# Kernel tuning notes

Measured on AMD Instinct MI355X. Metric: run time of the kernel, lower is better.

Reference implementation:

```python
import jax, jax.numpy as jnp
import numpy as np

H = 1024   # hidden_dim
B = 4096   # batch
T = 128    # forecast_len
IN = 1     # output_dim (univariate)


def setup_inputs() -> dict:
    key = jax.random.key(0)
    ks = jax.random.split(key, 8)
    s = 1.0 / np.sqrt(H)  # torch LSTM/Linear default uniform init scale
    u = lambda k, shape: jax.random.uniform(k, shape, jnp.float32, -s, s)
    return {
        "hidden": jax.random.normal(ks[0], (1, B, H), jnp.float32),
        "cell":   jax.random.normal(ks[1], (1, B, H), jnp.float32),
        "W_ih":   u(ks[2], (4 * H, IN)),   # torch gate order: i, f, g, o
        "W_hh":   u(ks[3], (4 * H, H)),
        "b_ih":   u(ks[4], (4 * H,)),
        "b_hh":   u(ks[5], (4 * H,)),
        "W_out":  u(ks[6], (IN, H)),
        "b_out":  u(ks[7], (IN,)),
    }


def reference(hidden, cell, W_ih, W_hh, b_ih, b_hh, W_out, b_out):
    h = hidden[0]  # [B, H]  (num_layers == 1)
    c = cell[0]    # [B, H]
    x0 = jnp.zeros((h.shape[0], IN), h.dtype)  # initial decoder input = zeros
    b = b_ih + b_hh

    def step(carry, _):
        x, h, c = carry
        gates = x @ W_ih.T + h @ W_hh.T + b          # [B, 4H]
        i, f, g, o = jnp.split(gates, 4, axis=-1)    # torch order i,f,g,o
        c = jax.nn.sigmoid(f) * c + jax.nn.sigmoid(i) * jnp.tanh(g)
        h = jax.nn.sigmoid(o) * jnp.tanh(c)
        pred = h @ W_out.T + b_out                   # [B, 1]
        return (pred, h, c), pred                    # prediction fed back as next input

    _, preds = jax.lax.scan(step, (x0, h, c), None, length=T)  # [T, B, 1]
    return jnp.transpose(preds, (1, 0, 2))  # [B, T, 1]
```

## Files before the change

### kernel.cpp

```cpp
#include <hip/hip_runtime.h>
#include <hip/hip_bf16.h>
#include <stdint.h>


#define HH 1024
#define BB 4096
#define TT 128

#define BM 128
#define BJ 32
#define BKK 64

typedef __bf16 bf16;
typedef __bf16 v8bf __attribute__((ext_vector_type(8)));
typedef float f32x4 __attribute__((ext_vector_type(4)));

__device__ __forceinline__ float fast_sigmoid(float x) {
    return 1.0f / (1.0f + __expf(-x));
}
__device__ __forceinline__ float fast_tanh(float x) {
    return 1.0f - 2.0f / (__expf(2.0f * x) + 1.0f);
}

__device__ __forceinline__ void gload_lds16(const void* g, void* l) {
    __builtin_amdgcn_global_load_lds(
        (const __attribute__((address_space(1))) uint32_t*)(uintptr_t)g,
        (__attribute__((address_space(3))) uint32_t*)(uint32_t)(uintptr_t)l,
        16, 0, 0);
}


__global__ void prep_weights(const float* __restrict__ Whh,
                             const float* __restrict__ bih,
                             const float* __restrict__ bhh,
                             bf16* __restrict__ Wr,
                             float* __restrict__ bias) {
    int idx = blockIdx.x * blockDim.x + threadIdx.x;
    if (idx < 4 * HH * HH) {
        int k   = idx & (HH - 1);
        int row = idx >> 10;
        int jb  = row >> 7;
        int g   = (row >> 5) & 3;
        int jj  = row & 31;
        int srow = g * HH + jb * 32 + jj;
        Wr[idx] = (bf16)Whh[srow * HH + k];
    }
    if (idx < 4 * HH) bias[idx] = bih[idx] + bhh[idx];
}

__global__ void prep_h(const float* __restrict__ h0, bf16* __restrict__ hb) {
    int idx = blockIdx.x * blockDim.x + threadIdx.x;
    if (idx < BB * HH) hb[idx] = (bf16)h0[idx];
}

__global__ void prep_pred(float* __restrict__ predbuf, const float* __restrict__ b_out) {
    int idx = blockIdx.x * blockDim.x + threadIdx.x;
    if (idx < (TT + 1) * BB) predbuf[idx] = (idx < BB) ? 0.0f : b_out[0];
}


__global__ __launch_bounds__(256, 4)
void lstm_step(const bf16* __restrict__ hread, bf16* __restrict__ hwrite,
               const float* __restrict__ cin, float* __restrict__ cout,
               const bf16* __restrict__ Wr, const float* __restrict__ bias,
               const float* __restrict__ Wih, const float* __restrict__ Wout,
               const float* __restrict__ predbuf_r, float* __restrict__ predbuf_w) {
    __shared__ bf16 As[BM][BKK];
    __shared__ bf16 Bs[BM][BKK];

    const int tid   = threadIdx.x;
    const int lane  = tid & 63;
    const int w     = tid >> 6;
    const int waveM = w >> 1, waveN = w & 1;
    const int quad  = lane >> 4, l15 = lane & 15;

    const int bid    = blockIdx.x;
    const int jb     = (bid & 7) * 4 + ((bid >> 3) & 3);
    const int blockB = (bid >> 5) * BM;

    f32x4 acc[4][4];
#pragma unroll
    for (int mi = 0; mi < 4; mi++)
#pragma unroll
        for (int g = 0; g < 4; g++) acc[mi][g] = (f32x4){0.f, 0.f, 0.f, 0.f};

    const bf16* Asrc = hread + (size_t)blockB * HH;
    const bf16* Bsrc = Wr + (size_t)jb * 128 * HH;

    const int r8 = lane >> 3;
    const int gc = (lane & 7) ^ r8;
    const int swr = l15 & 7;

    for (int k0 = 0; k0 < HH; k0 += BKK) {
#pragma unroll
        for (int c2 = 0; c2 < 4; c2++) {
            const int rowb = w * 32 + c2 * 8;
            gload_lds16(Asrc + (size_t)(rowb + r8) * HH + k0 + gc * 8, &As[rowb][0]);
            gload_lds16(Bsrc + (size_t)(rowb + r8) * HH + k0 + gc * 8, &Bs[rowb][0]);
        }
        asm volatile("s_waitcnt vmcnt(0)" ::: "memory");
        __syncthreads();
#pragma unroll
        for (int kk = 0; kk < 2; kk++) {
            v8bf a[4], b[4];
            const int pch = ((kk * 4 + quad) ^ swr) * 8;
#pragma unroll
            for (int mi = 0; mi < 4; mi++)
                a[mi] = *(const v8bf*)&As[waveM * 64 + mi * 16 + l15][pch];
#pragma unroll
            for (int g = 0; g < 4; g++)
                b[g] = *(const v8bf*)&Bs[g * 32 + waveN * 16 + l15][pch];
#pragma unroll
            for (int mi = 0; mi < 4; mi++)
#pragma unroll
                for (int g = 0; g < 4; g++)
                    acc[mi][g] = __builtin_amdgcn_mfma_f32_16x16x32_bf16(
                        a[mi], b[g], acc[mi][g], 0, 0, 0);
        }
        __syncthreads();
    }

    const int jj = jb * 32 + waveN * 16 + l15;
    float wih[4], bsv[4];
#pragma unroll
    for (int g = 0; g < 4; g++) {
        wih[g] = Wih[g * HH + jj];
        bsv[g] = bias[g * HH + jj];
    }
    const float wo = Wout[jj];

#pragma unroll
    for (int mi = 0; mi < 4; mi++) {
#pragma unroll
        for (int r = 0; r < 4; r++) {
            const int b = blockB + waveM * 64 + mi * 16 + quad * 4 + r;
            const float x = predbuf_r[b];
            const float gi = acc[mi][0][r] + x * wih[0] + bsv[0];
            const float gf = acc[mi][1][r] + x * wih[1] + bsv[1];
            const float gg = acc[mi][2][r] + x * wih[2] + bsv[2];
            const float go = acc[mi][3][r] + x * wih[3] + bsv[3];
            const float cn = fast_sigmoid(gf) * cin[(size_t)b * HH + jj]
                           + fast_sigmoid(gi) * fast_tanh(gg);
            cout[(size_t)b * HH + jj] = cn;
            const float hn = fast_sigmoid(go) * fast_tanh(cn);
            hwrite[(size_t)b * HH + jj] = (bf16)hn;
            float p = hn * wo;
            p += __shfl_xor(p, 1);
            p += __shfl_xor(p, 2);
            p += __shfl_xor(p, 4);
            p += __shfl_xor(p, 8);
            if (l15 == 0) atomicAdd(&predbuf_w[b], p);
        }
    }
}


__global__ void write_out(const float* __restrict__ predbuf, float* __restrict__ out) {
    int idx = blockIdx.x * blockDim.x + threadIdx.x;
    if (idx < BB * TT) {
        int t = idx & (TT - 1);
        int b = idx >> 7;
        out[idx] = predbuf[(size_t)(t + 1) * BB + b];
    }
}


extern "C" void kernel_launch(void* const* d_in, const int* in_sizes, int n_in,
                              void* d_out, int out_size, void* d_ws, size_t ws_size,
                              hipStream_t stream) {
    const float* hidden = (const float*)d_in[0];
    const float* cell   = (const float*)d_in[1];
    const float* Wih    = (const float*)d_in[2];
    const float* Whh    = (const float*)d_in[3];
    const float* bih    = (const float*)d_in[4];
    const float* bhh    = (const float*)d_in[5];
    const float* Wout   = (const float*)d_in[6];
    const float* bout   = (const float*)d_in[7];
    float* out = (float*)d_out;

    char* ws = (char*)d_ws;
    bf16* Wr = (bf16*)ws;        ws += (size_t)4 * HH * HH * 2;
    bf16* hb0 = (bf16*)ws;       ws += (size_t)BB * HH * 2;
    bf16* hb1 = (bf16*)ws;       ws += (size_t)BB * HH * 2;
    float* cbuf = (float*)ws;    ws += (size_t)BB * HH * 4;
    float* bias = (float*)ws;    ws += (size_t)4 * HH * 4;
    float* predbuf = (float*)ws; ws += (size_t)(TT + 1) * BB * 4;

    prep_weights<<<(4 * HH * HH + 255) / 256, 256, 0, stream>>>(Whh, bih, bhh, Wr, bias);
    prep_h<<<(BB * HH + 255) / 256, 256, 0, stream>>>(hidden, hb0);
    prep_pred<<<((TT + 1) * BB + 255) / 256, 256, 0, stream>>>(predbuf, bout);

    bf16* hb[2] = {hb0, hb1};
    for (int t = 0; t < TT; t++) {
        const bf16* hr = hb[t & 1];
        bf16* hw = hb[(t + 1) & 1];
        const float* ci = (t == 0) ? cell : cbuf;
        lstm_step<<<(HH / BJ) * (BB / BM), 256, 0, stream>>>(
            hr, hw, ci, cbuf, Wr, bias, Wih, Wout,
            predbuf + (size_t)t * BB, predbuf + (size_t)(t + 1) * BB);
    }

    write_out<<<(BB * TT + 255) / 256, 256, 0, stream>>>(predbuf, out);
}
```

Measured before the change: 5.765 ms.

## Widen LSTM step tile to 64 hidden units and use 32x32x16 MFMA

Each block now computes 128 batch rows by 64 hidden units across all four gates, so the B tile is 256 rows. The weights are re-permuted to match, and the grid shrinks from 1024 to 512 blocks. The inner product switches from 16x16x32 to 32x32x16 bf16 MFMA with 16-wide accumulators, and the epilogue row mapping and shuffle reduction are widened to 32 lanes. The aim is to cut how often each block reloads the h tile and to issue fewer, larger MFMA instructions. In exchange it needs more LDS and registers, lowers occupancy to 2 blocks per SIMD, and launches fewer blocks per step.

```diff
diff --git a/kernel.cpp b/kernel.cpp
--- a/kernel.cpp
+++ b/kernel.cpp
@@ -8,12 +8,11 @@
 #define TT 128
 
 #define BM 128
-#define BJ 32
 #define BKK 64
 
 typedef __bf16 bf16;
 typedef __bf16 v8bf __attribute__((ext_vector_type(8)));
-typedef float f32x4 __attribute__((ext_vector_type(4)));
+typedef float f32x16 __attribute__((ext_vector_type(16)));
 
 __device__ __forceinline__ float fast_sigmoid(float x) {
     return 1.0f / (1.0f + __expf(-x));
@@ -39,10 +38,11 @@
     if (idx < 4 * HH * HH) {
         int k   = idx & (HH - 1);
         int row = idx >> 10;
-        int jb  = row >> 7;
+        int jb2 = row >> 8;
+        int h   = (row >> 7) & 1;
         int g   = (row >> 5) & 3;
         int jj  = row & 31;
-        int srow = g * HH + jb * 32 + jj;
+        int srow = g * HH + jb2 * 64 + h * 32 + jj;
         Wr[idx] = (bf16)Whh[srow * HH + k];
     }
     if (idx < 4 * HH) bias[idx] = bih[idx] + bhh[idx];
@@ -59,68 +59,75 @@
 }
 
 
-__global__ __launch_bounds__(256, 4)
+__global__ __launch_bounds__(256, 2)
 void lstm_step(const bf16* __restrict__ hread, bf16* __restrict__ hwrite,
                const float* __restrict__ cin, float* __restrict__ cout,
                const bf16* __restrict__ Wr, const float* __restrict__ bias,
                const float* __restrict__ Wih, const float* __restrict__ Wout,
                const float* __restrict__ predbuf_r, float* __restrict__ predbuf_w) {
     __shared__ bf16 As[BM][BKK];
-    __shared__ bf16 Bs[BM][BKK];
+    __shared__ bf16 Bs[2 * BM][BKK];
 
     const int tid   = threadIdx.x;
     const int lane  = tid & 63;
     const int w     = tid >> 6;
     const int waveM = w >> 1, waveN = w & 1;
-    const int quad  = lane >> 4, l15 = lane & 15;
-
-    const int bid    = blockIdx.x;
-    const int jb     = (bid & 7) * 4 + ((bid >> 3) & 3);
-    const int blockB = (bid >> 5) * BM;
-
-    f32x4 acc[4][4];
-#pragma unroll
-    for (int mi = 0; mi < 4; mi++)
-#pragma unroll
-        for (int g = 0; g < 4; g++) acc[mi][g] = (f32x4){0.f, 0.f, 0.f, 0.f};
+    const int l31   = lane & 31, l5 = lane >> 5;
+
+    const int bid = blockIdx.x;
+    const int x8  = bid & 7;
+    const int i64 = bid >> 3;
+    const int jb2 = (x8 >> 1) * 4 + (i64 & 3);
+    const int bb  = (x8 & 1) * 16 + (i64 >> 2);
+    const int blockB = bb * BM;
+
+    f32x16 acc[2][4];
+#pragma unroll
+    for (int mi = 0; mi < 2; mi++)
+#pragma unroll
+        for (int g = 0; g < 4; g++) acc[mi][g] = (f32x16)(0.0f);
 
     const bf16* Asrc = hread + (size_t)blockB * HH;
-    const bf16* Bsrc = Wr + (size_t)jb * 128 * HH;
-
-    const int r8 = lane >> 3;
-    const int gc = (lane & 7) ^ r8;
-    const int swr = l15 & 7;
+    const bf16* Bsrc = Wr + (size_t)jb2 * 256 * HH;
+
+    const int r8  = lane >> 3;
+    const int gc  = (lane & 7) ^ r8;
+    const int swr = lane & 7;
 
     for (int k0 = 0; k0 < HH; k0 += BKK) {
 #pragma unroll
         for (int c2 = 0; c2 < 4; c2++) {
             const int rowb = w * 32 + c2 * 8;
             gload_lds16(Asrc + (size_t)(rowb + r8) * HH + k0 + gc * 8, &As[rowb][0]);
+        }
+#pragma unroll
+        for (int c2 = 0; c2 < 8; c2++) {
+            const int rowb = w * 64 + c2 * 8;
             gload_lds16(Bsrc + (size_t)(rowb + r8) * HH + k0 + gc * 8, &Bs[rowb][0]);
         }
         asm volatile("s_waitcnt vmcnt(0)" ::: "memory");
         __syncthreads();
 #pragma unroll
-        for (int kk = 0; kk < 2; kk++) {
-            v8bf a[4], b[4];
-            const int pch = ((kk * 4 + quad) ^ swr) * 8;
-#pragma unroll
-            for (int mi = 0; mi < 4; mi++)
-                a[mi] = *(const v8bf*)&As[waveM * 64 + mi * 16 + l15][pch];
+        for (int ks = 0; ks < 4; ks++) {
+            const int pch = ((ks * 2 + l5) ^ swr) * 8;
+            v8bf a[2], b[4];
+#pragma unroll
+            for (int mi = 0; mi < 2; mi++)
+                a[mi] = *(const v8bf*)&As[waveM * 64 + mi * 32 + l31][pch];
 #pragma unroll
             for (int g = 0; g < 4; g++)
-                b[g] = *(const v8bf*)&Bs[g * 32 + waveN * 16 + l15][pch];
-#pragma unroll
-            for (int mi = 0; mi < 4; mi++)
+                b[g] = *(const v8bf*)&Bs[waveN * 128 + g * 32 + l31][pch];
+#pragma unroll
+            for (int mi = 0; mi < 2; mi++)
 #pragma unroll
                 for (int g = 0; g < 4; g++)
-                    acc[mi][g] = __builtin_amdgcn_mfma_f32_16x16x32_bf16(
+                    acc[mi][g] = __builtin_amdgcn_mfma_f32_32x32x16_bf16(
                         a[mi], b[g], acc[mi][g], 0, 0, 0);
         }
         __syncthreads();
     }
 
-    const int jj = jb * 32 + waveN * 16 + l15;
+    const int jj = jb2 * 64 + waveN * 32 + l31;
     float wih[4], bsv[4];
 #pragma unroll
     for (int g = 0; g < 4; g++) {
@@ -130,26 +137,31 @@
     const float wo = Wout[jj];
 
 #pragma unroll
-    for (int mi = 0; mi < 4; mi++) {
-#pragma unroll
-        for (int r = 0; r < 4; r++) {
-            const int b = blockB + waveM * 64 + mi * 16 + quad * 4 + r;
-            const float x = predbuf_r[b];
-            const float gi = acc[mi][0][r] + x * wih[0] + bsv[0];
-            const float gf = acc[mi][1][r] + x * wih[1] + bsv[1];
-            const float gg = acc[mi][2][r] + x * wih[2] + bsv[2];
-            const float go = acc[mi][3][r] + x * wih[3] + bsv[3];
-            const float cn = fast_sigmoid(gf) * cin[(size_t)b * HH + jj]
-                           + fast_sigmoid(gi) * fast_tanh(gg);
-            cout[(size_t)b * HH + jj] = cn;
-            const float hn = fast_sigmoid(go) * fast_tanh(cn);
-            hwrite[(size_t)b * HH + jj] = (bf16)hn;
-            float p = hn * wo;
-            p += __shfl_xor(p, 1);
-            p += __shfl_xor(p, 2);
-            p += __shfl_xor(p, 4);
-            p += __shfl_xor(p, 8);
-            if (l15 == 0) atomicAdd(&predbuf_w[b], p);
+    for (int mi = 0; mi < 2; mi++) {
+#pragma unroll
+        for (int q = 0; q < 4; q++) {
+#pragma unroll
+            for (int s = 0; s < 4; s++) {
+                const int reg = q * 4 + s;
+                const int b = blockB + waveM * 64 + mi * 32 + s + 8 * q + 4 * l5;
+                const float x = predbuf_r[b];
+                const float gi = acc[mi][0][reg] + x * wih[0] + bsv[0];
+                const float gf = acc[mi][1][reg] + x * wih[1] + bsv[1];
+                const float gg = acc[mi][2][reg] + x * wih[2] + bsv[2];
+                const float go = acc[mi][3][reg] + x * wih[3] + bsv[3];
+                const float cn = fast_sigmoid(gf) * cin[(size_t)b * HH + jj]
+                               + fast_sigmoid(gi) * fast_tanh(gg);
+                cout[(size_t)b * HH + jj] = cn;
+                const float hn = fast_sigmoid(go) * fast_tanh(cn);
+                hwrite[(size_t)b * HH + jj] = (bf16)hn;
+                float p = hn * wo;
+                p += __shfl_xor(p, 1);
+                p += __shfl_xor(p, 2);
+                p += __shfl_xor(p, 4);
+                p += __shfl_xor(p, 8);
+                p += __shfl_xor(p, 16);
+                if (l31 == 0) atomicAdd(&predbuf_w[b], p);
+            }
         }
     }
 }
@@ -195,7 +207,7 @@
         const bf16* hr = hb[t & 1];
         bf16* hw = hb[(t + 1) & 1];
         const float* ci = (t == 0) ? cell : cbuf;
-        lstm_step<<<(HH / BJ) * (BB / BM), 256, 0, stream>>>(
+        lstm_step<<<512, 256, 0, stream>>>(
             hr, hw, ci, cbuf, Wr, bias, Wih, Wout,
             predbuf + (size_t)t * BB, predbuf + (size_t)(t + 1) * BB);
     }
```

After: 7.287 ms. +26.4%, slower.
